# Kernel optimization log

Measured on AMD Instinct MI355X. Metric: run time of the kernel, lower is better.

The kernel has to match this reference:

```python
import jax, jax.numpy as jnp
import numpy as np

NUM_ELEMENTS = 14
FLUID_ELEMS = (0, 3, 4, 10, 11)  # empty, water, gas, lava, acid
B, C, H, W = 16, 20, 512, 512


def setup_inputs() -> dict:
    key = jax.random.key(0)
    ks = jax.random.split(key, 6)
    # world: element one-hot channels + density + gravity + momentum + velocity + extra
    elem_ids = jax.random.randint(ks[0], (B, H, W), 0, NUM_ELEMENTS)
    onehot = jax.nn.one_hot(elem_ids, NUM_ELEMENTS, dtype=jnp.float32)  # [B,H,W,NE]
    onehot = jnp.transpose(onehot, (0, 3, 1, 2))
    density = jax.random.uniform(ks[1], (B, 1, H, W), dtype=jnp.float32) * 4.0
    gravity = (jax.random.uniform(ks[2], (B, 1, H, W)) > 0.2).astype(jnp.float32)
    rest = jax.random.normal(ks[3], (B, C - NUM_ELEMENTS - 2, H, W), dtype=jnp.float32)
    world = jnp.concatenate([onehot, density, gravity, rest], axis=1)
    rk = jax.random.split(ks[4], 4)
    return {
        "world": world,
        "rand_movement": jax.random.uniform(rk[0], (B, 1, H, W), dtype=jnp.float32),
        "rand_interact": jax.random.uniform(rk[1], (B, 1, H, W), dtype=jnp.float32),
        "rand_element": jax.random.uniform(rk[2], (B, 1, H, W), dtype=jnp.float32),
        "velocity_field": jax.random.normal(rk[3], (B, 2, H, W), dtype=jnp.float32),
        "did_gravity": jax.random.normal(ks[5], (B, 1, H, W), dtype=jnp.float32),
    }


def _fluid_flow(world, rand_movement, did_gravity):
    dens_c, grav_c, fm_c = NUM_ELEMENTS, NUM_ELEMENTS + 1, NUM_ELEMENTS + 2
    new_fm = jnp.zeros_like(world[:, :1])
    not_did_gravity = did_gravity <= 0
    for elem in FLUID_ELEMS:
        for fall_left in (True, False):
            sh = 1 if fall_left else -1
            gdir = lambda x, s=sh: jnp.roll(x, s, axis=3)      # toward fall direction
            gnot = lambda x, s=sh: jnp.roll(x, -s, axis=3)     # opposite direction
            # momentum channel is a live view of world in the torch code -> re-read
            fall_dir = (rand_movement + world[:, fm_c:fm_c + 1] + new_fm) > 0.5
            is_element = world[:, elem:elem + 1] == 1
            is_right_element = gnot(is_element)
            density = world[:, dens_c:dens_c + 1]
            is_matching_fall = fall_dir if fall_left else ~fall_dir
            is_right_matching_fall = gnot(is_matching_fall)
            is_left_density_lower = (density - gdir(density)) > 0
            is_right_density_higher = (gnot(density) - density) > 0
            is_gravity = world[:, grav_c:grav_c + 1] == 1
            is_left_gravity = gdir(is_gravity) & is_gravity
            is_right_gravity = gnot(is_gravity) & is_gravity
            becomes_left = (is_matching_fall & is_element & not_did_gravity
                            & is_left_density_lower & is_left_gravity)
            becomes_right = (is_right_matching_fall & is_right_element & gnot(not_did_gravity)
                             & is_right_density_higher & is_right_gravity)
            new_fm = new_fm + becomes_right.astype(world.dtype) * (2.0 if fall_left else -2.0)
            a = becomes_left.astype(world.dtype)
            b = becomes_right.astype(world.dtype)
            # interp2: (~a & ~b)*world + a*world_left + b*world_right
            world = (1.0 - a) * (1.0 - b) * world + a * gdir(world) + b * gnot(world)
    world = world.at[:, fm_c:fm_c + 1].set(new_fm)
    return world


def reference(world, rand_movement, rand_interact, rand_element, velocity_field, did_gravity):
    world = _fluid_flow(world, rand_movement, did_gravity)
    return (world, rand_movement, rand_interact, rand_element, velocity_field, did_gravity)
```

## Files before the change

### kernel.cpp

```cpp
#include <hip/hip_runtime.h>


#define CCH 20
#define BHW ((size_t)4194304)
#define CH  ((size_t)262144)

#define LD8(dst, p) { const float4* _q=(const float4*)(p); float4 _x=_q[0],_y=_q[1]; \
  dst[0]=_x.x;dst[1]=_x.y;dst[2]=_x.z;dst[3]=_x.w;dst[4]=_y.x;dst[5]=_y.y;dst[6]=_y.z;dst[7]=_y.w; }
#define ST8(p, v) { float4* _q=(float4*)(p); _q[0]=make_float4(v[0],v[1],v[2],v[3]); \
  _q[1]=make_float4(v[4],v[5],v[6],v[7]); }

__global__ __launch_bounds__(256) void fluid_wave_kernel(
    const float* __restrict__ world_in,
    const float* __restrict__ rm_in,
    const float* __restrict__ ri_in,
    const float* __restrict__ re_in,
    const float* __restrict__ vf_in,
    const float* __restrict__ dg_in,
    float* __restrict__ out)
{
    const int lane = threadIdx.x & 63;
    const int row  = (blockIdx.x << 2) + (threadIdx.x >> 6);
    const int b    = row >> 9;
    const int h    = row & 511;
    const int px0  = lane << 3;

    const size_t srow = (size_t)row * 512;
    const size_t wrow = (((size_t)b * CCH) * 512 + h) * 512;
    const size_t vrow0 = (((size_t)b * 2) * 512 + h) * 512;
    const size_t vrow1 = vrow0 + CH;

    float t[8];
    LD8(t, ri_in + srow + px0); ST8(out + 21*BHW + srow + px0, t);
    LD8(t, re_in + srow + px0); ST8(out + 22*BHW + srow + px0, t);
    LD8(t, vf_in + vrow0 + px0); ST8(out + 23*BHW + vrow0 + px0, t);
    LD8(t, vf_in + vrow1 + px0); ST8(out + 23*BHW + vrow1 + px0, t);

    float rm[8], dgv[8], dens[8], fm[8], nf[8];
    uint32_t code[8], sA[8], sB[8];
    LD8(rm,  rm_in + srow + px0);  ST8(out + 20*BHW + srow + px0, rm);
    LD8(dgv, dg_in + srow + px0);  ST8(out + 25*BHW + srow + px0, dgv);
    LD8(dens, world_in + wrow + 14*CH + px0);
    LD8(fm,   world_in + wrow + 16*CH + px0);

    uint32_t ndgm = 0;
    #pragma unroll
    for (int j = 0; j < 8; ++j) ndgm |= (uint32_t)(dgv[j] <= 0.0f) << j;

    LD8(t, world_in + wrow + 15*CH + px0);
    #pragma unroll
    for (int j = 0; j < 8; ++j) code[j] = (uint32_t)(t[j] == 1.0f) << 20;
    LD8(t, world_in + wrow +  0*CH + px0);
    #pragma unroll
    for (int j = 0; j < 8; ++j) code[j] |= (uint32_t)(t[j] == 1.0f);
    LD8(t, world_in + wrow +  3*CH + px0);
    #pragma unroll
    for (int j = 0; j < 8; ++j) code[j] |= (uint32_t)(t[j] == 1.0f) << 4;
    LD8(t, world_in + wrow +  4*CH + px0);
    #pragma unroll
    for (int j = 0; j < 8; ++j) code[j] |= (uint32_t)(t[j] == 1.0f) << 8;
    LD8(t, world_in + wrow + 10*CH + px0);
    #pragma unroll
    for (int j = 0; j < 8; ++j) code[j] |= (uint32_t)(t[j] == 1.0f) << 12;
    LD8(t, world_in + wrow + 11*CH + px0);
    #pragma unroll
    for (int j = 0; j < 8; ++j) code[j] |= (uint32_t)(t[j] == 1.0f) << 16;

    #pragma unroll
    for (int j = 0; j < 8; ++j) {
        sA[j] = 1u | ((uint32_t)(px0 + j) << 4);
        sB[j] = 0u;
        nf[j] = 0.0f;
    }

    const int lft = (lane + 63) & 63, rgt = (lane + 1) & 63;

    #pragma unroll 1
    for (int ei = 0; ei < 5; ++ei) {
        const int sft = ei * 4;
        #pragma unroll
        for (int fi = 0; fi < 2; ++fi) {
            const bool  fl = (fi == 0);
            const float k  = fl ? 2.0f : -2.0f;

            const float dL = __shfl(dens[7], lft), dR = __shfl(dens[0], rgt);
            const float fL = __shfl(fm[7],  lft), fR = __shfl(fm[0],  rgt);
            const uint32_t cL = (uint32_t)__shfl((int)code[7], lft);
            const uint32_t cR = (uint32_t)__shfl((int)code[0], rgt);
            const uint32_t AL = (uint32_t)__shfl((int)sA[7], lft);
            const uint32_t AR = (uint32_t)__shfl((int)sA[0], rgt);
            const uint32_t BL = (uint32_t)__shfl((int)sB[7], lft);
            const uint32_t BR = (uint32_t)__shfl((int)sB[0], rgt);

            uint32_t am = 0;
            #pragma unroll
            for (int j = 0; j < 8; ++j) {
                float dwm; uint32_t cwm;
                if (fl) { dwm = j ? dens[j-1] : dL;       cwm = j ? code[j-1] : cL; }
                else    { dwm = (j<7) ? dens[j+1] : dR;   cwm = (j<7) ? code[j+1] : cR; }
                const bool fd  = ((rm[j] + fm[j]) + nf[j]) > 0.5f;
                const bool imf = fl ? fd : !fd;
                const bool a = imf
                    && (((code[j] >> sft) & 15u) == 1u)
                    && (((ndgm >> j) & 1u) != 0u)
                    && ((dens[j] - dwm) > 0.0f)
                    && (((cwm    >> 20) & 15u) == 1u)
                    && (((code[j] >> 20) & 15u) == 1u);
                am |= (uint32_t)a << j;
            }

            const uint32_t aLm = (uint32_t)__shfl((int)am, lft);
            const uint32_t aRm = (uint32_t)__shfl((int)am, rgt);
            const uint32_t bm = fl ? ((am >> 1) | ((aRm & 1u) << 7))
                                   : (((am << 1) & 0xFFu) | ((aLm >> 7) & 1u));

            float prD = dL, prF = fL;
            uint32_t prC = cL, prA = AL, prB = BL;
            #pragma unroll
            for (int j = 0; j < 8; ++j) {
                const float    ahD = (j<7) ? dens[j+1] : dR;
                const float    ahF = (j<7) ? fm[j+1]   : fR;
                const uint32_t ahC = (j<7) ? code[j+1] : cR;
                const uint32_t ahA = (j<7) ? sA[j+1]   : AR;
                const uint32_t ahB = (j<7) ? sB[j+1]   : BR;
                const float    wmD = fl ? prD : ahD, wpD = fl ? ahD : prD;
                const float    wmF = fl ? prF : ahF, wpF = fl ? ahF : prF;
                const uint32_t wmC = fl ? prC : ahC, wpC = fl ? ahC : prC;
                const uint32_t wmA = fl ? prA : ahA, wpA = fl ? ahA : prA;
                const uint32_t wmB = fl ? prB : ahB, wpB = fl ? ahB : prB;
                const bool a  = (am >> j) & 1u;
                const bool bb = (bm >> j) & 1u;
                if (bb) nf[j] += k;
                prD = dens[j]; prF = fm[j]; prC = code[j]; prA = sA[j]; prB = sB[j];
                if (a & bb) {
                    dens[j] = wmD + wpD; fm[j] = wmF + wpF; code[j] = wmC + wpC;
                    const uint32_t c1 = wmA & 15u, c2 = wpA & 15u;
                    const uint64_t l1 = ((uint64_t)(wmA >> 4)) | ((uint64_t)wmB << 27);
                    const uint64_t l2 = ((uint64_t)(wpA >> 4)) | ((uint64_t)wpB << 27);
                    uint32_t cnt = c1 + c2; if (cnt > 6u) cnt = 6u;
                    const uint64_t all = l1 | (l2 << (9u * c1));
                    sA[j] = cnt | ((uint32_t)(all & 0x7FFFFFFull) << 4);
                    sB[j] = (uint32_t)((all >> 27) & 0x7FFFFFFull);
                } else if (a) {
                    dens[j] = wmD; fm[j] = wmF; code[j] = wmC; sA[j] = wmA; sB[j] = wmB;
                } else if (bb) {
                    dens[j] = wpD; fm[j] = wpF; code[j] = wpC; sA[j] = wpA; sB[j] = wpB;
                }
            }
        }
    }

    float o[8];
    #pragma unroll
    for (int j=0;j<8;++j) o[j] = (float)( code[j]        & 15u); ST8(out + wrow +  0*CH + px0, o);
    #pragma unroll
    for (int j=0;j<8;++j) o[j] = (float)((code[j] >>  4) & 15u); ST8(out + wrow +  3*CH + px0, o);
    #pragma unroll
    for (int j=0;j<8;++j) o[j] = (float)((code[j] >>  8) & 15u); ST8(out + wrow +  4*CH + px0, o);
    #pragma unroll
    for (int j=0;j<8;++j) o[j] = (float)((code[j] >> 12) & 15u); ST8(out + wrow + 10*CH + px0, o);
    #pragma unroll
    for (int j=0;j<8;++j) o[j] = (float)((code[j] >> 16) & 15u); ST8(out + wrow + 11*CH + px0, o);
    #pragma unroll
    for (int j=0;j<8;++j) o[j] = (float)((code[j] >> 20) & 15u); ST8(out + wrow + 15*CH + px0, o);
    ST8(out + wrow + 14*CH + px0, dens);
    ST8(out + wrow + 16*CH + px0, nf);

    const int GC[12] = {1,2,5,6,7,8,9,12,13,17,18,19};
    #pragma unroll
    for (int g = 0; g < 12; ++g) {
        const float* src = world_in + wrow + (size_t)GC[g] * CH;
        float v[8];
        #pragma unroll
        for (int j = 0; j < 8; ++j) {
            const uint32_t A = sA[j], c = A & 15u;
            float x = src[(A >> 4) & 511u];
            if (c > 1u) { x += src[(A >> 13) & 511u];
              if (c > 2u) { x += src[(A >> 22) & 511u];
                if (c > 3u) { const uint32_t Bv = sB[j]; x += src[Bv & 511u];
                  if (c > 4u) { x += src[(Bv >> 9) & 511u];
                    if (c > 5u) x += src[(Bv >> 18) & 511u]; } } } }
            v[j] = x;
        }
        ST8(out + wrow + (size_t)GC[g] * CH + px0, v);
    }
}

extern "C" void kernel_launch(void* const* d_in, const int* in_sizes, int n_in,
                              void* d_out, int out_size, void* d_ws, size_t ws_size,
                              hipStream_t stream) {
    const float* world = (const float*)d_in[0];
    const float* rm    = (const float*)d_in[1];
    const float* ri    = (const float*)d_in[2];
    const float* re    = (const float*)d_in[3];
    const float* vf    = (const float*)d_in[4];
    const float* dg    = (const float*)d_in[5];
    float* out = (float*)d_out;

    dim3 grid(2048), block(256);
    fluid_wave_kernel<<<grid, block, 0, stream>>>(world, rm, ri, re, vf, dg, out);
}
```

Before: 224.7 us.

## Stage passive channel rows in LDS for gather instead of global indexed loads

The 12 passive world channels were previously gathered with per-pixel indexed global loads using the tracked source positions. Each wave now loads every channel row coalesced, writes it to padded, double-buffered shared memory, and gathers from LDS. The next channel's load is prefetched while the current one is gathered. Extra source taps are handled only when some pixel in the wave has a multi-source count. This removes scattered global gathers at the cost of LDS traffic, padding arithmetic and more register pressure.

```diff
diff --git a/kernel.cpp b/kernel.cpp
--- a/kernel.cpp
+++ b/kernel.cpp
@@ -19,20 +19,23 @@
     const float* __restrict__ dg_in,
     float* __restrict__ out)
 {
+    __shared__ float s_g[4][2][528];
+
     const int lane = threadIdx.x & 63;
-    const int row  = (blockIdx.x << 2) + (threadIdx.x >> 6);
+    const int wv   = threadIdx.x >> 6;
+    const int row  = (blockIdx.x << 2) + wv;
     const int b    = row >> 9;
     const int h    = row & 511;
     const int px0  = lane << 3;
 
-    const size_t srow = (size_t)row * 512;
-    const size_t wrow = (((size_t)b * CCH) * 512 + h) * 512;
+    const size_t srow  = (size_t)row * 512;
+    const size_t wrow  = (((size_t)b * CCH) * 512 + h) * 512;
     const size_t vrow0 = (((size_t)b * 2) * 512 + h) * 512;
     const size_t vrow1 = vrow0 + CH;
 
     float t[8];
-    LD8(t, ri_in + srow + px0); ST8(out + 21*BHW + srow + px0, t);
-    LD8(t, re_in + srow + px0); ST8(out + 22*BHW + srow + px0, t);
+    LD8(t, ri_in + srow + px0);  ST8(out + 21*BHW + srow + px0, t);
+    LD8(t, re_in + srow + px0);  ST8(out + 22*BHW + srow + px0, t);
     LD8(t, vf_in + vrow0 + px0); ST8(out + 23*BHW + vrow0 + px0, t);
     LD8(t, vf_in + vrow1 + px0); ST8(out + 23*BHW + vrow1 + px0, t);
 
@@ -65,6 +68,9 @@
     LD8(t, world_in + wrow + 11*CH + px0);
     #pragma unroll
     for (int j = 0; j < 8; ++j) code[j] |= (uint32_t)(t[j] == 1.0f) << 16;
+
+    float cur[8];
+    LD8(cur, world_in + wrow + 1*CH + px0);
 
     #pragma unroll
     for (int j = 0; j < 8; ++j) {
@@ -166,23 +172,42 @@
     ST8(out + wrow + 14*CH + px0, dens);
     ST8(out + wrow + 16*CH + px0, nf);
 
-    const int GC[12] = {1,2,5,6,7,8,9,12,13,17,18,19};
+    uint32_t multi = 0;
+    int sidx0[8];
+    #pragma unroll
+    for (int j = 0; j < 8; ++j) {
+        const uint32_t p = (sA[j] >> 4) & 511u;
+        sidx0[j] = (int)(p + (p >> 5));
+        multi |= (uint32_t)((sA[j] & 15u) > 1u) << j;
+    }
+    const int pad = lane >> 2;
+
+    static const int GCv[12] = {1,2,5,6,7,8,9,12,13,17,18,19};
+    float nxt[8];
     #pragma unroll
     for (int g = 0; g < 12; ++g) {
-        const float* src = world_in + wrow + (size_t)GC[g] * CH;
+        float* buf = &s_g[wv][g & 1][0];
+        #pragma unroll
+        for (int j = 0; j < 8; ++j) buf[px0 + pad + j] = cur[j];
+        if (g < 11) { LD8(nxt, world_in + wrow + (size_t)GCv[g + 1] * CH + px0); }
         float v[8];
         #pragma unroll
-        for (int j = 0; j < 8; ++j) {
-            const uint32_t A = sA[j], c = A & 15u;
-            float x = src[(A >> 4) & 511u];
-            if (c > 1u) { x += src[(A >> 13) & 511u];
-              if (c > 2u) { x += src[(A >> 22) & 511u];
-                if (c > 3u) { const uint32_t Bv = sB[j]; x += src[Bv & 511u];
-                  if (c > 4u) { x += src[(Bv >> 9) & 511u];
-                    if (c > 5u) x += src[(Bv >> 18) & 511u]; } } } }
-            v[j] = x;
+        for (int j = 0; j < 8; ++j) v[j] = buf[sidx0[j]];
+        if (multi) {
+            #pragma unroll
+            for (int j = 0; j < 8; ++j) if ((multi >> j) & 1u) {
+                const uint32_t A = sA[j], c = A & 15u, Bv = sB[j];
+                uint32_t p1 = (A >> 13) & 511u; float x = v[j] + buf[p1 + (p1 >> 5)];
+                if (c > 2u) { uint32_t p2 = (A >> 22) & 511u; x += buf[p2 + (p2 >> 5)];
+                  if (c > 3u) { uint32_t p3 = Bv & 511u; x += buf[p3 + (p3 >> 5)];
+                    if (c > 4u) { uint32_t p4 = (Bv >> 9) & 511u; x += buf[p4 + (p4 >> 5)];
+                      if (c > 5u) { uint32_t p5 = (Bv >> 18) & 511u; x += buf[p5 + (p5 >> 5)]; } } } }
+                v[j] = x;
+            }
         }
-        ST8(out + wrow + (size_t)GC[g] * CH + px0, v);
+        ST8(out + wrow + (size_t)GCv[g] * CH + px0, v);
+        #pragma unroll
+        for (int j = 0; j < 8; ++j) cur[j] = nxt[j];
     }
 }
 
```

Measured after the change: 181.2 us. 1.24x faster.
